# Kernel tuning notes

Hardware: AMD Instinct MI355X
Metric: run time of the kernel (lower is better)

## Reference

```python
import jax, jax.numpy as jnp
import numpy as np

N_NODES = 50000
N_EDGES = 800000
IN_C, HID_C, OUT_C = 128, 128, 64


def setup_inputs() -> dict:
    key = jax.random.key(0)
    ks = jax.random.split(key, 8)
    x = jax.random.normal(ks[0], (N_NODES, IN_C), dtype=jnp.float32)
    edge_index = jax.random.randint(ks[1], (2, N_EDGES), 0, N_NODES, dtype=jnp.int64)
    def glorot(k, shape):
        lim = np.sqrt(6.0 / (shape[0] + shape[1])).astype(np.float32)
        return jax.random.uniform(k, shape, jnp.float32, -lim, lim)
    return {
        "x": x,
        "edge_index": edge_index,
        "W1l": glorot(ks[2], (IN_C, HID_C)),
        "b1": jnp.zeros((HID_C,), jnp.float32),
        "W1r": glorot(ks[3], (IN_C, HID_C)),
        "W2l": glorot(ks[4], (HID_C, OUT_C)),
        "b2": jnp.zeros((OUT_C,), jnp.float32),
        "W2r": glorot(ks[5], (HID_C, OUT_C)),
    }


def _sage_conv(h, src, dst, Wl, bl, Wr):
    # mean aggregation over incoming edges (source -> target)
    n = h.shape[0]
    msg_sum = jax.ops.segment_sum(h[src], dst, num_segments=n)          # [N, d]
    deg = jax.ops.segment_sum(jnp.ones((src.shape[0],), h.dtype), dst, num_segments=n)
    agg = msg_sum / jnp.maximum(deg, 1.0)[:, None]                      # zero-degree -> 0
    # lin_l(agg) + lin_r(h); lin_l carries the bias (PyG SAGEConv default)
    return agg @ Wl + bl + h @ Wr


def reference(x, edge_index, W1l, b1, W1r, W2l, b2, W2r):
    src, dst = edge_index[0], edge_index[1]
    h = jax.nn.relu(_sage_conv(x, src, dst, W1l, b1, W1r))
    # eval-mode forward: dropout is identity
    out = _sage_conv(h, src, dst, W2l, b2, W2r)
    return out
```

## Files before the change

### kernel.cpp

```cpp
#include <hip/hip_runtime.h>

#define N_NODES 50000
#define N_EDGES 800000
#define IN_C    128
#define HID_C   128
#define OUT_C   64
#define NBUCK   196
#define BCAP    6144
#define EPB     2048
#define EBLKS   ((N_EDGES + EPB - 1) / EPB)
#define PACK_BLKS 192
#define MM1_BLKS  ((N_NODES + 63) / 64)

typedef unsigned short ushort_t;
typedef unsigned int   uint_t;
typedef unsigned char  uchar_t;
typedef __attribute__((ext_vector_type(8))) short bf16x8;
typedef __attribute__((ext_vector_type(4))) float f32x4;
typedef __attribute__((ext_vector_type(2))) float f32x2;

__device__ inline ushort_t f2bf(float f) {
    uint_t u = __float_as_uint(f);
    uint_t r = (u + 0x7fffu + ((u >> 16) & 1u)) >> 16;
    return (ushort_t)r;
}
__device__ inline float bflo(uint_t v) { return __uint_as_float(v << 16); }
__device__ inline float bfhi(uint_t v) { return __uint_as_float(v & 0xffff0000u); }

__device__ inline void pack_one(const float* W, ushort_t* Wp, int K, int N, int idx) {
    const int j  = idx & 7;
    const int L  = (idx >> 3) & 63;
    const int t  = idx >> 9;
    const int KT = K / 32;
    const int kt = t % KT;
    const int ct = t / KT;
    const int k  = kt * 32 + (L >> 4) * 8 + j;
    const int n  = ct * 16 + (L & 15);
    Wp[idx] = f2bf(W[k * N + n]);
}

__global__ __launch_bounds__(256) void k0_kernel(
    const float* __restrict__ W1l, const float* __restrict__ W1r,
    const float* __restrict__ W2l, const float* __restrict__ W2r,
    ushort_t* __restrict__ wpack, int* __restrict__ gcur)
{
    const int b = blockIdx.x;
    if (b < PACK_BLKS) {
        const int tid = b * 256 + threadIdx.x;
        if (tid < 16384)      pack_one(W1l, wpack,          IN_C,  HID_C, tid);
        else if (tid < 32768) pack_one(W1r, wpack + 16384,  IN_C,  HID_C, tid - 16384);
        else if (tid < 40960) pack_one(W2l, wpack + 32768,  HID_C, OUT_C, tid - 32768);
        else if (tid < 49152) pack_one(W2r, wpack + 40960,  HID_C, OUT_C, tid - 40960);
    } else {
        if (threadIdx.x < NBUCK) gcur[threadIdx.x] = 0;
    }
}

__device__ inline void mm1_body(int bid, const float* __restrict__ x,
                                const ushort_t* __restrict__ wpack,
                                uchar_t* __restrict__ p1f, ushort_t* __restrict__ t1b)
{
    const int wave = threadIdx.x >> 6;
    const int lane = threadIdx.x & 63;
    const int quad = lane >> 4;
    const int m    = lane & 15;
    const int row0 = bid * 64 + wave * 16;
    const int arow = min(row0 + m, N_NODES - 1);

    const bf16x8* Bl = (const bf16x8*)(wpack);
    const bf16x8* Br = (const bf16x8*)(wpack + 16384);

    f32x4 accl[8], accr[8];
#pragma unroll
    for (int ct = 0; ct < 8; ++ct) { accl[ct] = (f32x4)(0.0f); accr[ct] = (f32x4)(0.0f); }

#pragma unroll
    for (int kt = 0; kt < 4; ++kt) {
        const float* xp = x + (size_t)arow * IN_C + kt * 32 + quad * 8;
        const float4 a0 = *(const float4*)(xp);
        const float4 a1 = *(const float4*)(xp + 4);
        bf16x8 af;
        af[0] = (short)f2bf(a0.x); af[1] = (short)f2bf(a0.y);
        af[2] = (short)f2bf(a0.z); af[3] = (short)f2bf(a0.w);
        af[4] = (short)f2bf(a1.x); af[5] = (short)f2bf(a1.y);
        af[6] = (short)f2bf(a1.z); af[7] = (short)f2bf(a1.w);
#pragma unroll
        for (int ct = 0; ct < 8; ++ct) {
            const bf16x8 bl = Bl[(ct * 4 + kt) * 64 + lane];
            const bf16x8 br = Br[(ct * 4 + kt) * 64 + lane];
            accl[ct] = __builtin_amdgcn_mfma_f32_16x16x32_bf16(af, bl, accl[ct], 0, 0, 0);
            accr[ct] = __builtin_amdgcn_mfma_f32_16x16x32_bf16(af, br, accr[ct], 0, 0, 0);
        }
    }

#pragma unroll
    for (int r = 0; r < 4; ++r) {
        const int orow = row0 + quad * 4 + r;
        if (orow < N_NODES) {
#pragma unroll
            for (int ct = 0; ct < 8; ++ct) {
                const int col = ct * 16 + m;
                const float v = accl[ct][r];
                const int pk = __builtin_amdgcn_cvt_pk_fp8_f32(v, v, 0, false);
                p1f[(size_t)orow * HID_C + col] = (uchar_t)(pk & 0xff);
                t1b[(size_t)orow * HID_C + col] = f2bf(accr[ct][r]);
            }
        }
    }
}

__global__ __launch_bounds__(256) void k1_kernel(
    const float* __restrict__ x, const ushort_t* __restrict__ wpack,
    uchar_t* __restrict__ p1f, ushort_t* __restrict__ t1b,
    const int* __restrict__ src, const int* __restrict__ dst,
    int* gcur, int* __restrict__ ebuf)
{
    __shared__ int lh[256], gbase[256], lcur[256];
    const int b = blockIdx.x;
    if (b < MM1_BLKS) {
        mm1_body(b, x, wpack, p1f, t1b);
        return;
    }
    const int blk = b - MM1_BLKS;
    const int t = threadIdx.x;
    lh[t] = 0;
    __syncthreads();
    const int base = blk * EPB;
    int v8[8], b8[8];
#pragma unroll
    for (int j = 0; j < 8; ++j) {
        const int e = base + t + j * 256;
        if (e < N_EDGES) {
            const int s = src[e], d = dst[e];
            b8[j] = d >> 8;
            v8[j] = (s << 8) | (d & 255);
            atomicAdd(&lh[b8[j]], 1);
        } else b8[j] = -1;
    }
    __syncthreads();
    if (t < NBUCK) {
        const int run = lh[t];
        gbase[t] = (run > 0) ? atomicAdd(&gcur[t], run) : 0;
        lcur[t] = 0;
    }
    __syncthreads();
#pragma unroll
    for (int j = 0; j < 8; ++j) {
        const int bk = b8[j];
        if (bk >= 0) {
            const int p = atomicAdd(&lcur[bk], 1);
            ebuf[bk * BCAP + gbase[bk] + p] = v8[j];
        }
    }
}

__global__ __launch_bounds__(256) void fill_kernel(
    const int* __restrict__ ebuf, const int* __restrict__ gcur,
    int* __restrict__ cnt, int* __restrict__ row_ptr, int* __restrict__ csr)
{
    __shared__ int lh[256], loff[256], lcur[256];
    const int b = blockIdx.x;
    const int t = threadIdx.x;
    const int e0 = b * BCAP;
    const int nb = gcur[b];
    lh[t] = 0;
    __syncthreads();
    for (int i = t; i < nb; i += 256) atomicAdd(&lh[ebuf[e0 + i] & 255], 1);
    __syncthreads();
    const int v = lh[t];
    loff[t] = v;
    __syncthreads();
    for (int off = 1; off < 256; off <<= 1) {
        const int add = (t >= off) ? loff[t - off] : 0;
        __syncthreads();
        loff[t] += add;
        __syncthreads();
    }
    const int ex = loff[t] - v;
    const int node = b * 256 + t;
    if (node < N_NODES) { cnt[node] = v; row_ptr[node] = e0 + ex; }
    lcur[t] = ex;
    __syncthreads();
    for (int i = t; i < nb; i += 256) {
        const int pr = ebuf[e0 + i];
        const int p = atomicAdd(&lcur[pr & 255], 1);
        csr[e0 + p] = pr >> 8;
    }
}

__global__ __launch_bounds__(256) void agg1_kernel(
    const uchar_t* __restrict__ p1f, const ushort_t* __restrict__ t1b,
    const float* __restrict__ b1, const int* __restrict__ row_ptr,
    const int* __restrict__ cnt, const int* __restrict__ csr,
    ushort_t* __restrict__ hb)
{
    const int wave = threadIdx.x >> 6;
    const int half = (threadIdx.x >> 5) & 1;
    const int c4   = threadIdx.x & 31;
    const int node = blockIdx.x * 8 + wave * 2 + half;
    const int start = row_ptr[node];
    const int degi  = cnt[node];
    const uint_t* p1u = (const uint_t*)p1f;

    float a0 = 0.0f, a1 = 0.0f, a2 = 0.0f, a3 = 0.0f;
    int e = 0;
    for (; e + 3 < degi; e += 4) {
        const int s0 = csr[start + e];
        const int s1 = csr[start + e + 1];
        const int s2 = csr[start + e + 2];
        const int s3 = csr[start + e + 3];
        const uint_t v0 = p1u[(size_t)s0 * 32 + c4];
        const uint_t v1 = p1u[(size_t)s1 * 32 + c4];
        const uint_t v2 = p1u[(size_t)s2 * 32 + c4];
        const uint_t v3 = p1u[(size_t)s3 * 32 + c4];
        const f32x2 l0 = __builtin_amdgcn_cvt_pk_f32_fp8((int)v0, false);
        const f32x2 h0 = __builtin_amdgcn_cvt_pk_f32_fp8((int)v0, true);
        const f32x2 l1 = __builtin_amdgcn_cvt_pk_f32_fp8((int)v1, false);
        const f32x2 h1 = __builtin_amdgcn_cvt_pk_f32_fp8((int)v1, true);
        const f32x2 l2 = __builtin_amdgcn_cvt_pk_f32_fp8((int)v2, false);
        const f32x2 h2 = __builtin_amdgcn_cvt_pk_f32_fp8((int)v2, true);
        const f32x2 l3 = __builtin_amdgcn_cvt_pk_f32_fp8((int)v3, false);
        const f32x2 h3 = __builtin_amdgcn_cvt_pk_f32_fp8((int)v3, true);
        a0 += l0.x + l1.x + l2.x + l3.x;
        a1 += l0.y + l1.y + l2.y + l3.y;
        a2 += h0.x + h1.x + h2.x + h3.x;
        a3 += h0.y + h1.y + h2.y + h3.y;
    }
    for (; e < degi; ++e) {
        const uint_t v0 = p1u[(size_t)csr[start + e] * 32 + c4];
        const f32x2 l0 = __builtin_amdgcn_cvt_pk_f32_fp8((int)v0, false);
        const f32x2 h0 = __builtin_amdgcn_cvt_pk_f32_fp8((int)v0, true);
        a0 += l0.x; a1 += l0.y; a2 += h0.x; a3 += h0.y;
    }

    const float inv = 1.0f / fmaxf((float)degi, 1.0f);
    const size_t i = (size_t)node * HID_C + c4 * 4;
    const uint2 tv = *(const uint2*)(t1b + i);
    const float4 bv = *(const float4*)(b1 + c4 * 4);
    const float r0 = fmaxf(fmaf(a0, inv, bv.x + bflo(tv.x)), 0.0f);
    const float r1 = fmaxf(fmaf(a1, inv, bv.y + bfhi(tv.x)), 0.0f);
    const float r2 = fmaxf(fmaf(a2, inv, bv.z + bflo(tv.y)), 0.0f);
    const float r3 = fmaxf(fmaf(a3, inv, bv.w + bfhi(tv.y)), 0.0f);
    uint2 o;
    o.x = (uint_t)f2bf(r0) | ((uint_t)f2bf(r1) << 16);
    o.y = (uint_t)f2bf(r2) | ((uint_t)f2bf(r3) << 16);
    *(uint2*)(hb + i) = o;
}

__global__ __launch_bounds__(256) void mm2_mfma(
    const ushort_t* __restrict__ hb,
    const ushort_t* __restrict__ wpack,
    ushort_t* __restrict__ p2b, ushort_t* __restrict__ t2b)
{
    const int wave = threadIdx.x >> 6;
    const int lane = threadIdx.x & 63;
    const int quad = lane >> 4;
    const int m    = lane & 15;
    const int row0 = blockIdx.x * 64 + wave * 16;
    const int arow = min(row0 + m, N_NODES - 1);

    const bf16x8* Bl = (const bf16x8*)(wpack + 32768);
    const bf16x8* Br = (const bf16x8*)(wpack + 40960);

    f32x4 accl[4], accr[4];
#pragma unroll
    for (int ct = 0; ct < 4; ++ct) { accl[ct] = (f32x4)(0.0f); accr[ct] = (f32x4)(0.0f); }

#pragma unroll
    for (int kt = 0; kt < 4; ++kt) {
        const bf16x8 af = *(const bf16x8*)(hb + (size_t)arow * HID_C + kt * 32 + quad * 8);
#pragma unroll
        for (int ct = 0; ct < 4; ++ct) {
            const bf16x8 bl = Bl[(ct * 4 + kt) * 64 + lane];
            const bf16x8 br = Br[(ct * 4 + kt) * 64 + lane];
            accl[ct] = __builtin_amdgcn_mfma_f32_16x16x32_bf16(af, bl, accl[ct], 0, 0, 0);
            accr[ct] = __builtin_amdgcn_mfma_f32_16x16x32_bf16(af, br, accr[ct], 0, 0, 0);
        }
    }

#pragma unroll
    for (int r = 0; r < 4; ++r) {
        const int orow = row0 + quad * 4 + r;
        if (orow < N_NODES) {
#pragma unroll
            for (int ct = 0; ct < 4; ++ct) {
                const int col = ct * 16 + m;
                p2b[(size_t)orow * OUT_C + col] = f2bf(accl[ct][r]);
                t2b[(size_t)orow * OUT_C + col] = f2bf(accr[ct][r]);
            }
        }
    }
}

__global__ __launch_bounds__(256) void agg2_kernel(
    const ushort_t* __restrict__ p2b, const ushort_t* __restrict__ t2b,
    const float* __restrict__ b2, const int* __restrict__ row_ptr,
    const int* __restrict__ cnt, const int* __restrict__ csr,
    float* __restrict__ out)
{
    const int wave = threadIdx.x >> 6;
    const int half = (threadIdx.x >> 5) & 1;
    const int c2   = threadIdx.x & 31;
    const int node = blockIdx.x * 8 + wave * 2 + half;
    const int start = row_ptr[node];
    const int degi  = cnt[node];
    const uint_t* p2u = (const uint_t*)p2b;

    float a0 = 0.0f, a1 = 0.0f;
    int e = 0;
    for (; e + 3 < degi; e += 4) {
        const int s0 = csr[start + e];
        const int s1 = csr[start + e + 1];
        const int s2 = csr[start + e + 2];
        const int s3 = csr[start + e + 3];
        const uint_t v0 = p2u[(size_t)s0 * 32 + c2];
        const uint_t v1 = p2u[(size_t)s1 * 32 + c2];
        const uint_t v2 = p2u[(size_t)s2 * 32 + c2];
        const uint_t v3 = p2u[(size_t)s3 * 32 + c2];
        a0 += bflo(v0) + bflo(v1) + bflo(v2) + bflo(v3);
        a1 += bfhi(v0) + bfhi(v1) + bfhi(v2) + bfhi(v3);
    }
    for (; e < degi; ++e) {
        const uint_t v0 = p2u[(size_t)csr[start + e] * 32 + c2];
        a0 += bflo(v0); a1 += bfhi(v0);
    }

    const float inv = 1.0f / fmaxf((float)degi, 1.0f);
    const size_t i = (size_t)node * OUT_C + c2 * 2;
    const uint_t tv = *(const uint_t*)(t2b + i);
    const float2 bv = *(const float2*)(b2 + c2 * 2);
    float2 o;
    o.x = fmaf(a0, inv, bv.x + bflo(tv));
    o.y = fmaf(a1, inv, bv.y + bfhi(tv));
    *(float2*)(out + i) = o;
}

extern "C" void kernel_launch(void* const* d_in, const int* in_sizes, int n_in,
                              void* d_out, int out_size, void* d_ws, size_t ws_size,
                              hipStream_t stream)
{
    const float* x   = (const float*)d_in[0];
    const int*   ei  = (const int*)d_in[1];
    const float* W1l = (const float*)d_in[2];
    const float* b1  = (const float*)d_in[3];
    const float* W1r = (const float*)d_in[4];
    const float* W2l = (const float*)d_in[5];
    const float* b2  = (const float*)d_in[6];
    const float* W2r = (const float*)d_in[7];
    float* out = (float*)d_out;

    const int* src = ei;
    const int* dst = ei + N_EDGES;

    const size_t NH = (size_t)N_NODES * HID_C;
    const size_t NO = (size_t)N_NODES * OUT_C;
    const size_t EB = (size_t)NBUCK * BCAP;

    char* ws = (char*)d_ws;
    ushort_t* t1b   = (ushort_t*)ws;                   ws += NH * sizeof(ushort_t);
    ushort_t* hb    = (ushort_t*)ws;                   ws += NH * sizeof(ushort_t);
    ushort_t* t2b   = (ushort_t*)ws;                   ws += NO * sizeof(ushort_t);
    ushort_t* p2b   = (ushort_t*)ws;                   ws += NO * sizeof(ushort_t);
    ushort_t* wpack = (ushort_t*)ws;                   ws += 49152 * sizeof(ushort_t);
    int* ebuf    = (int*)ws;                           ws += EB * sizeof(int);
    int* csr     = (int*)ws;                           ws += EB * sizeof(int);
    int* cnt     = (int*)ws;                           ws += N_NODES * sizeof(int);
    int* row_ptr = (int*)ws;                           ws += N_NODES * sizeof(int);
    int* gcur    = (int*)ws;                           ws += NBUCK * sizeof(int);
    uchar_t* p1f = (uchar_t*)ws;                       ws += NH * sizeof(uchar_t);

    const size_t need = (size_t)(ws - (char*)d_ws);
    if (ws_size < need) return;

    k0_kernel<<<PACK_BLKS + 1, 256, 0, stream>>>(W1l, W1r, W2l, W2r, wpack, gcur);
    k1_kernel<<<MM1_BLKS + EBLKS, 256, 0, stream>>>(
        x, wpack, p1f, t1b, src, dst, gcur, ebuf);
    fill_kernel<<<NBUCK, 256, 0, stream>>>(ebuf, gcur, cnt, row_ptr, csr);

    agg1_kernel<<<N_NODES / 8, 256, 0, stream>>>(p1f, t1b, b1, row_ptr, cnt, csr, hb);
    mm2_mfma<<<MM1_BLKS, 256, 0, stream>>>(hb, wpack, p2b, t2b);
    agg2_kernel<<<N_NODES / 8, 256, 0, stream>>>(p2b, t2b, b2, row_ptr, cnt, csr, out);
}
```

Measured before the change: 181.5 us.

## Fuse layer-1 aggregation with layer-2 MFMA matmul via shared memory

Merges the layer-1 mean aggregation kernel and the layer-2 MFMA matmul into one kernel. Each block aggregates 64 nodes into a padded LDS tile and then runs the matmul from LDS, so the bf16 hidden activations are never written to or read back from global memory and one launch is removed. Both gather kernels now have 16 lanes per node with 8-byte loads instead of 32 lanes with 4-byte loads, giving 4 nodes per wave. The cost is a block-wide barrier between the irregular gather and the matmul, and fewer nodes in flight per block during the gather.

```diff
diff --git a/kernel.cpp b/kernel.cpp
--- a/kernel.cpp
+++ b/kernel.cpp
@@ -11,6 +11,7 @@
 #define EBLKS   ((N_EDGES + EPB - 1) / EPB)
 #define PACK_BLKS 192
 #define MM1_BLKS  ((N_NODES + 63) / 64)
+#define HS_STRIDE 136
 
 typedef unsigned short ushort_t;
 typedef unsigned int   uint_t;
@@ -188,19 +189,135 @@
     }
 }
 
-__global__ __launch_bounds__(256) void agg1_kernel(
+__global__ __launch_bounds__(256) void l2f_kernel(
     const uchar_t* __restrict__ p1f, const ushort_t* __restrict__ t1b,
     const float* __restrict__ b1, const int* __restrict__ row_ptr,
     const int* __restrict__ cnt, const int* __restrict__ csr,
-    ushort_t* __restrict__ hb)
-{
-    const int wave = threadIdx.x >> 6;
-    const int half = (threadIdx.x >> 5) & 1;
-    const int c4   = threadIdx.x & 31;
-    const int node = blockIdx.x * 8 + wave * 2 + half;
+    const ushort_t* __restrict__ wpack,
+    ushort_t* __restrict__ p2b, ushort_t* __restrict__ t2b)
+{
+    __shared__ ushort_t hs[64 * HS_STRIDE];
+    const int blk = blockIdx.x;
+    const int wv  = threadIdx.x >> 6;
+    const int g   = (threadIdx.x >> 4) & 3;
+    const int c8  = threadIdx.x & 15;
+    const uint2* p1v = (const uint2*)p1f;
+
+#pragma unroll
+    for (int p = 0; p < 4; ++p) {
+        const int nl   = p * 16 + wv * 4 + g;
+        const int node = blk * 64 + nl;
+        float a0=0,a1=0,a2=0,a3=0,a4=0,a5=0,a6=0,a7=0;
+        int degi = 0;
+        if (node < N_NODES) {
+            const int start = row_ptr[node];
+            degi = cnt[node];
+            int e = 0;
+            for (; e + 3 < degi; e += 4) {
+                const int s0 = csr[start + e];
+                const int s1 = csr[start + e + 1];
+                const int s2 = csr[start + e + 2];
+                const int s3 = csr[start + e + 3];
+                const uint2 v0 = p1v[(size_t)s0 * 16 + c8];
+                const uint2 v1 = p1v[(size_t)s1 * 16 + c8];
+                const uint2 v2 = p1v[(size_t)s2 * 16 + c8];
+                const uint2 v3 = p1v[(size_t)s3 * 16 + c8];
+#pragma unroll
+                for (int q = 0; q < 4; ++q) {
+                    const uint2 v = (q == 0) ? v0 : (q == 1) ? v1 : (q == 2) ? v2 : v3;
+                    const f32x2 lx = __builtin_amdgcn_cvt_pk_f32_fp8((int)v.x, false);
+                    const f32x2 hx = __builtin_amdgcn_cvt_pk_f32_fp8((int)v.x, true);
+                    const f32x2 ly = __builtin_amdgcn_cvt_pk_f32_fp8((int)v.y, false);
+                    const f32x2 hy = __builtin_amdgcn_cvt_pk_f32_fp8((int)v.y, true);
+                    a0 += lx.x; a1 += lx.y; a2 += hx.x; a3 += hx.y;
+                    a4 += ly.x; a5 += ly.y; a6 += hy.x; a7 += hy.y;
+                }
+            }
+            for (; e < degi; ++e) {
+                const uint2 v = p1v[(size_t)csr[start + e] * 16 + c8];
+                const f32x2 lx = __builtin_amdgcn_cvt_pk_f32_fp8((int)v.x, false);
+                const f32x2 hx = __builtin_amdgcn_cvt_pk_f32_fp8((int)v.x, true);
+                const f32x2 ly = __builtin_amdgcn_cvt_pk_f32_fp8((int)v.y, false);
+                const f32x2 hy = __builtin_amdgcn_cvt_pk_f32_fp8((int)v.y, true);
+                a0 += lx.x; a1 += lx.y; a2 += hx.x; a3 += hx.y;
+                a4 += ly.x; a5 += ly.y; a6 += hy.x; a7 += hy.y;
+            }
+        }
+        uint4 o = make_uint4(0u, 0u, 0u, 0u);
+        if (node < N_NODES) {
+            const float inv = 1.0f / fmaxf((float)degi, 1.0f);
+            const size_t i = (size_t)node * HID_C + c8 * 8;
+            const uint4 tv = *(const uint4*)(t1b + i);
+            const float4 bL = *(const float4*)(b1 + c8 * 8);
+            const float4 bH = *(const float4*)(b1 + c8 * 8 + 4);
+            const float r0 = fmaxf(fmaf(a0, inv, bL.x + bflo(tv.x)), 0.0f);
+            const float r1 = fmaxf(fmaf(a1, inv, bL.y + bfhi(tv.x)), 0.0f);
+            const float r2 = fmaxf(fmaf(a2, inv, bL.z + bflo(tv.y)), 0.0f);
+            const float r3 = fmaxf(fmaf(a3, inv, bL.w + bfhi(tv.y)), 0.0f);
+            const float r4 = fmaxf(fmaf(a4, inv, bH.x + bflo(tv.z)), 0.0f);
+            const float r5 = fmaxf(fmaf(a5, inv, bH.y + bfhi(tv.z)), 0.0f);
+            const float r6 = fmaxf(fmaf(a6, inv, bH.z + bflo(tv.w)), 0.0f);
+            const float r7 = fmaxf(fmaf(a7, inv, bH.w + bfhi(tv.w)), 0.0f);
+            o.x = (uint_t)f2bf(r0) | ((uint_t)f2bf(r1) << 16);
+            o.y = (uint_t)f2bf(r2) | ((uint_t)f2bf(r3) << 16);
+            o.z = (uint_t)f2bf(r4) | ((uint_t)f2bf(r5) << 16);
+            o.w = (uint_t)f2bf(r6) | ((uint_t)f2bf(r7) << 16);
+        }
+        *(uint4*)&hs[nl * HS_STRIDE + c8 * 8] = o;
+    }
+    __syncthreads();
+
+    const int lane = threadIdx.x & 63;
+    const int quad = lane >> 4;
+    const int m    = lane & 15;
+    const int row0 = blk * 64 + wv * 16;
+
+    const bf16x8* Bl = (const bf16x8*)(wpack + 32768);
+    const bf16x8* Br = (const bf16x8*)(wpack + 40960);
+
+    f32x4 accl[4], accr[4];
+#pragma unroll
+    for (int ct = 0; ct < 4; ++ct) { accl[ct] = (f32x4)(0.0f); accr[ct] = (f32x4)(0.0f); }
+
+#pragma unroll
+    for (int kt = 0; kt < 4; ++kt) {
+        const bf16x8 af = *(const bf16x8*)&hs[(wv * 16 + m) * HS_STRIDE + kt * 32 + quad * 8];
+#pragma unroll
+        for (int ct = 0; ct < 4; ++ct) {
+            const bf16x8 bl = Bl[(ct * 4 + kt) * 64 + lane];
+            const bf16x8 br = Br[(ct * 4 + kt) * 64 + lane];
+            accl[ct] = __builtin_amdgcn_mfma_f32_16x16x32_bf16(af, bl, accl[ct], 0, 0, 0);
+            accr[ct] = __builtin_amdgcn_mfma_f32_16x16x32_bf16(af, br, accr[ct], 0, 0, 0);
+        }
+    }
+
+#pragma unroll
+    for (int r = 0; r < 4; ++r) {
+        const int orow = row0 + quad * 4 + r;
+        if (orow < N_NODES) {
+#pragma unroll
+            for (int ct = 0; ct < 4; ++ct) {
+                const int col = ct * 16 + m;
+                p2b[(size_t)orow * OUT_C + col] = f2bf(accl[ct][r]);
+                t2b[(size_t)orow * OUT_C + col] = f2bf(accr[ct][r]);
+            }
+        }
+    }
+}
+
+__global__ __launch_bounds__(256) void agg2_kernel(
+    const ushort_t* __restrict__ p2b, const ushort_t* __restrict__ t2b,
+    const float* __restrict__ b2, const int* __restrict__ row_ptr,
+    const int* __restrict__ cnt, const int* __restrict__ csr,
+    float* __restrict__ out)
+{
+    const int wv  = threadIdx.x >> 6;
+    const int g   = (threadIdx.x >> 4) & 3;
+    const int c4  = threadIdx.x & 15;
+    const int node = blockIdx.x * 16 + wv * 4 + g;
     const int start = row_ptr[node];
     const int degi  = cnt[node];
-    const uint_t* p1u = (const uint_t*)p1f;
+    const uint2* p2v = (const uint2*)p2b;
 
     float a0 = 0.0f, a1 = 0.0f, a2 = 0.0f, a3 = 0.0f;
     int e = 0;
@@ -209,130 +326,31 @@
         const int s1 = csr[start + e + 1];
         const int s2 = csr[start + e + 2];
         const int s3 = csr[start + e + 3];
-        const uint_t v0 = p1u[(size_t)s0 * 32 + c4];
-        const uint_t v1 = p1u[(size_t)s1 * 32 + c4];
-        const uint_t v2 = p1u[(size_t)s2 * 32 + c4];
-        const uint_t v3 = p1u[(size_t)s3 * 32 + c4];
-        const f32x2 l0 = __builtin_amdgcn_cvt_pk_f32_fp8((int)v0, false);
-        const f32x2 h0 = __builtin_amdgcn_cvt_pk_f32_fp8((int)v0, true);
-        const f32x2 l1 = __builtin_amdgcn_cvt_pk_f32_fp8((int)v1, false);
-        const f32x2 h1 = __builtin_amdgcn_cvt_pk_f32_fp8((int)v1, true);
-        const f32x2 l2 = __builtin_amdgcn_cvt_pk_f32_fp8((int)v2, false);
-        const f32x2 h2 = __builtin_amdgcn_cvt_pk_f32_fp8((int)v2, true);
-        const f32x2 l3 = __builtin_amdgcn_cvt_pk_f32_fp8((int)v3, false);
-        const f32x2 h3 = __builtin_amdgcn_cvt_pk_f32_fp8((int)v3, true);
-        a0 += l0.x + l1.x + l2.x + l3.x;
-        a1 += l0.y + l1.y + l2.y + l3.y;
-        a2 += h0.x + h1.x + h2.x + h3.x;
-        a3 += h0.y + h1.y + h2.y + h3.y;
+        const uint2 v0 = p2v[(size_t)s0 * 16 + c4];
+        const uint2 v1 = p2v[(size_t)s1 * 16 + c4];
+        const uint2 v2 = p2v[(size_t)s2 * 16 + c4];
+        const uint2 v3 = p2v[(size_t)s3 * 16 + c4];
+        a0 += bflo(v0.x) + bflo(v1.x) + bflo(v2.x) + bflo(v3.x);
+        a1 += bfhi(v0.x) + bfhi(v1.x) + bfhi(v2.x) + bfhi(v3.x);
+        a2 += bflo(v0.y) + bflo(v1.y) + bflo(v2.y) + bflo(v3.y);
+        a3 += bfhi(v0.y) + bfhi(v1.y) + bfhi(v2.y) + bfhi(v3.y);
     }
     for (; e < degi; ++e) {
-        const uint_t v0 = p1u[(size_t)csr[start + e] * 32 + c4];
-        const f32x2 l0 = __builtin_amdgcn_cvt_pk_f32_fp8((int)v0, false);
-        const f32x2 h0 = __builtin_amdgcn_cvt_pk_f32_fp8((int)v0, true);
-        a0 += l0.x; a1 += l0.y; a2 += h0.x; a3 += h0.y;
+        const uint2 v0 = p2v[(size_t)csr[start + e] * 16 + c4];
+        a0 += bflo(v0.x); a1 += bfhi(v0.x);
+        a2 += bflo(v0.y); a3 += bfhi(v0.y);
     }
 
     const float inv = 1.0f / fmaxf((float)degi, 1.0f);
-    const size_t i = (size_t)node * HID_C + c4 * 4;
-    const uint2 tv = *(const uint2*)(t1b + i);
-    const float4 bv = *(const float4*)(b1 + c4 * 4);
-    const float r0 = fmaxf(fmaf(a0, inv, bv.x + bflo(tv.x)), 0.0f);
-    const float r1 = fmaxf(fmaf(a1, inv, bv.y + bfhi(tv.x)), 0.0f);
-    const float r2 = fmaxf(fmaf(a2, inv, bv.z + bflo(tv.y)), 0.0f);
-    const float r3 = fmaxf(fmaf(a3, inv, bv.w + bfhi(tv.y)), 0.0f);
-    uint2 o;
-    o.x = (uint_t)f2bf(r0) | ((uint_t)f2bf(r1) << 16);
-    o.y = (uint_t)f2bf(r2) | ((uint_t)f2bf(r3) << 16);
-    *(uint2*)(hb + i) = o;
-}
-
-__global__ __launch_bounds__(256) void mm2_mfma(
-    const ushort_t* __restrict__ hb,
-    const ushort_t* __restrict__ wpack,
-    ushort_t* __restrict__ p2b, ushort_t* __restrict__ t2b)
-{
-    const int wave = threadIdx.x >> 6;
-    const int lane = threadIdx.x & 63;
-    const int quad = lane >> 4;
-    const int m    = lane & 15;
-    const int row0 = blockIdx.x * 64 + wave * 16;
-    const int arow = min(row0 + m, N_NODES - 1);
-
-    const bf16x8* Bl = (const bf16x8*)(wpack + 32768);
-    const bf16x8* Br = (const bf16x8*)(wpack + 40960);
-
-    f32x4 accl[4], accr[4];
-#pragma unroll
-    for (int ct = 0; ct < 4; ++ct) { accl[ct] = (f32x4)(0.0f); accr[ct] = (f32x4)(0.0f); }
-
-#pragma unroll
-    for (int kt = 0; kt < 4; ++kt) {
-        const bf16x8 af = *(const bf16x8*)(hb + (size_t)arow * HID_C + kt * 32 + quad * 8);
-#pragma unroll
-        for (int ct = 0; ct < 4; ++ct) {
-            const bf16x8 bl = Bl[(ct * 4 + kt) * 64 + lane];
-            const bf16x8 br = Br[(ct * 4 + kt) * 64 + lane];
-            accl[ct] = __builtin_amdgcn_mfma_f32_16x16x32_bf16(af, bl, accl[ct], 0, 0, 0);
-            accr[ct] = __builtin_amdgcn_mfma_f32_16x16x32_bf16(af, br, accr[ct], 0, 0, 0);
-        }
-    }
-
-#pragma unroll
-    for (int r = 0; r < 4; ++r) {
-        const int orow = row0 + quad * 4 + r;
-        if (orow < N_NODES) {
-#pragma unroll
-            for (int ct = 0; ct < 4; ++ct) {
-                const int col = ct * 16 + m;
-                p2b[(size_t)orow * OUT_C + col] = f2bf(accl[ct][r]);
-                t2b[(size_t)orow * OUT_C + col] = f2bf(accr[ct][r]);
-            }
-        }
-    }
-}
-
-__global__ __launch_bounds__(256) void agg2_kernel(
-    const ushort_t* __restrict__ p2b, const ushort_t* __restrict__ t2b,
-    const float* __restrict__ b2, const int* __restrict__ row_ptr,
-    const int* __restrict__ cnt, const int* __restrict__ csr,
-    float* __restrict__ out)
-{
-    const int wave = threadIdx.x >> 6;
-    const int half = (threadIdx.x >> 5) & 1;
-    const int c2   = threadIdx.x & 31;
-    const int node = blockIdx.x * 8 + wave * 2 + half;
-    const int start = row_ptr[node];
-    const int degi  = cnt[node];
-    const uint_t* p2u = (const uint_t*)p2b;
-
-    float a0 = 0.0f, a1 = 0.0f;
-    int e = 0;
-    for (; e + 3 < degi; e += 4) {
-        const int s0 = csr[start + e];
-        const int s1 = csr[start + e + 1];
-        const int s2 = csr[start + e + 2];
-        const int s3 = csr[start + e + 3];
-        const uint_t v0 = p2u[(size_t)s0 * 32 + c2];
-        const uint_t v1 = p2u[(size_t)s1 * 32 + c2];
-        const uint_t v2 = p2u[(size_t)s2 * 32 + c2];
-        const uint_t v3 = p2u[(size_t)s3 * 32 + c2];
-        a0 += bflo(v0) + bflo(v1) + bflo(v2) + bflo(v3);
-        a1 += bfhi(v0) + bfhi(v1) + bfhi(v2) + bfhi(v3);
-    }
-    for (; e < degi; ++e) {
-        const uint_t v0 = p2u[(size_t)csr[start + e] * 32 + c2];
-        a0 += bflo(v0); a1 += bfhi(v0);
-    }
-
-    const float inv = 1.0f / fmaxf((float)degi, 1.0f);
-    const size_t i = (size_t)node * OUT_C + c2 * 2;
-    const uint_t tv = *(const uint_t*)(t2b + i);
-    const float2 bv = *(const float2*)(b2 + c2 * 2);
-    float2 o;
-    o.x = fmaf(a0, inv, bv.x + bflo(tv));
-    o.y = fmaf(a1, inv, bv.y + bfhi(tv));
-    *(float2*)(out + i) = o;
+    const size_t i = (size_t)node * OUT_C + c4 * 4;
+    const uint2 tv = *(const uint2*)(t2b + i);
+    const float4 bv = *(const float4*)(b2 + c4 * 4);
+    float4 o;
+    o.x = fmaf(a0, inv, bv.x + bflo(tv.x));
+    o.y = fmaf(a1, inv, bv.y + bfhi(tv.x));
+    o.z = fmaf(a2, inv, bv.z + bflo(tv.y));
+    o.w = fmaf(a3, inv, bv.w + bfhi(tv.y));
+    *(float4*)(out + i) = o;
 }
 
 extern "C" void kernel_launch(void* const* d_in, const int* in_sizes, int n_in,
@@ -358,7 +376,6 @@
 
     char* ws = (char*)d_ws;
     ushort_t* t1b   = (ushort_t*)ws;                   ws += NH * sizeof(ushort_t);
-    ushort_t* hb    = (ushort_t*)ws;                   ws += NH * sizeof(ushort_t);
     ushort_t* t2b   = (ushort_t*)ws;                   ws += NO * sizeof(ushort_t);
     ushort_t* p2b   = (ushort_t*)ws;                   ws += NO * sizeof(ushort_t);
     ushort_t* wpack = (ushort_t*)ws;                   ws += 49152 * sizeof(ushort_t);
@@ -376,8 +393,8 @@
     k1_kernel<<<MM1_BLKS + EBLKS, 256, 0, stream>>>(
         x, wpack, p1f, t1b, src, dst, gcur, ebuf);
     fill_kernel<<<NBUCK, 256, 0, stream>>>(ebuf, gcur, cnt, row_ptr, csr);
-
-    agg1_kernel<<<N_NODES / 8, 256, 0, stream>>>(p1f, t1b, b1, row_ptr, cnt, csr, hb);
-    mm2_mfma<<<MM1_BLKS, 256, 0, stream>>>(hb, wpack, p2b, t2b);
-    agg2_kernel<<<N_NODES / 8, 256, 0, stream>>>(p2b, t2b, b2, row_ptr, cnt, csr, out);
-}
+    l2f_kernel<<<MM1_BLKS, 256, 0, stream>>>(
+        p1f, t1b, b1, row_ptr, cnt, csr, wpack, p2b, t2b);
+    agg2_kernel<<<(N_NODES + 15) / 16, 256, 0, stream>>>(
+        p2b, t2b, b2, row_ptr, cnt, csr, out);
+}
```

New measurement: 177.2 us. -2.4%, faster.
